# Performance work log

Measured on AMD Instinct MI355X. Metric: run time of the kernel, lower is better.

Reference implementation:

```python
import jax, jax.numpy as jnp
import numpy as np

NUM_EMBEDDINGS = 4096
EMBEDDING_DIM = 256
COMMITMENT_COST = 0.25
DECAY = 0.99
EPS = 1e-5
NORM_EPS = 1e-6
B, T = 64, 1024


def _l2norm(x):
    # torch.nn.functional.normalize: x / max(||x||_2, eps)
    n = jnp.sqrt(jnp.sum(x * x, axis=-1, keepdims=True))
    return x / jnp.maximum(n, NORM_EPS)


def setup_inputs() -> dict:
    key = jax.random.key(0)
    k1, k2 = jax.random.split(key)
    z = jax.random.normal(k1, (B, EMBEDDING_DIM, T), dtype=jnp.float32)
    weight = jax.random.normal(k2, (NUM_EMBEDDINGS, EMBEDDING_DIM), dtype=jnp.float32)
    weight = weight.at[0].set(0.0)  # reserved zero code
    ema_cluster_size = jnp.zeros((NUM_EMBEDDINGS,), dtype=jnp.float32)
    ema_w = weight  # buffer initialized as a clone of the codebook
    return {"z": z, "weight": weight, "ema_cluster_size": ema_cluster_size, "ema_w": ema_w}


def reference(z, weight, ema_cluster_size, ema_w):
    K = weight.shape[0]
    zp = jnp.transpose(z, (0, 2, 1))            # [B, T, D]
    b, t, d = zp.shape
    flat_z = zp.reshape(-1, d)                  # [N, D]
    flat_z_norm = _l2norm(flat_z)
    weight_norm = _l2norm(weight)
    # cosine similarity; argmin(1 - cos) == argmax(cos); code 0 excluded via -inf
    cos_sim = jnp.einsum('nd,kd->nk', flat_z_norm, weight_norm)
    cos_sim = cos_sim.at[:, 0].set(-jnp.inf)
    idx = jnp.argmax(cos_sim, axis=1)           # [N] int
    q = weight[idx].reshape(zp.shape)           # [B, T, D]

    # --- training-mode EMA codebook update (buffer math, no grad) ---
    counts = jax.ops.segment_sum(jnp.ones_like(idx, dtype=flat_z.dtype), idx, num_segments=K)
    new_cs = DECAY * ema_cluster_size + (1.0 - DECAY) * counts
    dw = jax.ops.segment_sum(flat_z_norm, idx, num_segments=K)  # [K, D]
    new_ema_w = DECAY * ema_w + (1.0 - DECAY) * dw
    new_cs = new_cs.at[0].set(0.0)
    new_ema_w = new_ema_w.at[0].set(0.0)
    n = jnp.sum(new_cs)
    cluster_size = (new_cs + EPS) / (n + K * EPS) * n
    new_weight = _l2norm(new_ema_w / cluster_size[:, None])
    new_weight = new_weight.at[0].set(0.0)

    loss = COMMITMENT_COST * jnp.mean((jax.lax.stop_gradient(q) - zp) ** 2)
    quantized = zp + jax.lax.stop_gradient(q - zp)  # straight-through
    quantized = jnp.transpose(quantized, (0, 2, 1))  # back to [B, D, T]
    codes = idx.reshape(b, t)
    return quantized, loss, codes, new_weight, new_cs, new_ema_w
```

## Files before the change

### kernel.cpp

```cpp
#include <hip/hip_runtime.h>
#include <math.h>

#define NUM_K 4096
#define DIM   256
#define TLEN  1024
#define DT    (DIM * TLEN)
#define CAP   2048

typedef short bf16x8 __attribute__((ext_vector_type(8)));
typedef float f32x4  __attribute__((ext_vector_type(4)));

static __device__ __forceinline__ unsigned short f2bf(float x) {
  unsigned u = __float_as_uint(x);
  u += 0x7fffu + ((u >> 16) & 1u);
  return (unsigned short)(u >> 16);
}

static __device__ __forceinline__ f32x4 mfma16(bf16x8 a, bf16x8 b, f32x4 c) {
  return __builtin_amdgcn_mfma_f32_16x16x32_bf16(a, b, c, 0, 0, 0);
}

__global__ __launch_bounds__(256) void wnorm_kernel(const float* __restrict__ w,
                                                    float* __restrict__ wnorms) {
  const int k = blockIdx.x * 256 + threadIdx.x;
  const float* row = w + (size_t)k * DIM;
  float p[2];
#pragma unroll
  for (int blk = 0; blk < 2; ++blk) {
    const float* b = row + blk * 128;
    float r[8];
#pragma unroll
    for (int j = 0; j < 8; ++j) r[j] = __fmul_rn(b[j], b[j]);
    for (int i = 8; i < 128; i += 8) {
#pragma unroll
      for (int j = 0; j < 8; ++j) r[j] = __fadd_rn(r[j], __fmul_rn(b[i + j], b[i + j]));
    }
    p[blk] = __fadd_rn(__fadd_rn(__fadd_rn(r[0], r[1]), __fadd_rn(r[2], r[3])),
                       __fadd_rn(__fadd_rn(r[4], r[5]), __fadd_rn(r[6], r[7])));
  }
  wnorms[k] = fmaxf(__fsqrt_rn(__fadd_rn(p[0], p[1])), 1e-6f);
}

__global__ __launch_bounds__(256) void wnf32_kernel(const float* __restrict__ w,
                                                    const float* __restrict__ wnorms,
                                                    float* __restrict__ wnf) {
  const int idx = blockIdx.x * 256 + threadIdx.x;
  const float m = wnorms[idx >> 6];
  const float4 v = *reinterpret_cast<const float4*>(w + (size_t)idx * 4);
  float4 o;
  o.x = __fdiv_rn(v.x, m); o.y = __fdiv_rn(v.y, m);
  o.z = __fdiv_rn(v.z, m); o.w = __fdiv_rn(v.w, m);
  *reinterpret_cast<float4*>(wnf + (size_t)idx * 4) = o;
}

__global__ __launch_bounds__(256) void wfrag_kernel(const float* __restrict__ wnf,
                                                    unsigned short* __restrict__ img) {
  const int t = blockIdx.x * 256 + threadIdx.x;
  const int lane = t & 63;
  const int fragid = t >> 6;
  const int jg = fragid & 3;
  const int kb = (fragid >> 2) & 7;
  const int chunk = fragid >> 5;
  const int c  = (chunk << 6) + (jg << 4) + (lane & 15);
  const int d0 = (kb << 5) + ((lane >> 4) << 3);
  const float* src = wnf + (size_t)c * DIM + d0;
  union { bf16x8 v; unsigned short u[8]; } o;
#pragma unroll
  for (int u = 0; u < 8; ++u) o.u[u] = f2bf(src[u]);
  *reinterpret_cast<bf16x8*>(img + (size_t)fragid * 512 + lane * 8) = o.v;
}

__global__ __launch_bounds__(256, 2) void vq_main_kernel(
    const float* __restrict__ z, const float* __restrict__ weight,
    const unsigned short* __restrict__ wimg, const float* __restrict__ wnf32,
    float* __restrict__ znT, float* __restrict__ out_codes,
    float* __restrict__ counts, float* __restrict__ loss_accum) {
  __shared__ float pp[2][64];
  __shared__ float tnorm[64];
  __shared__ float v1p[2][64];
  __shared__ float thr[64];
  __shared__ int   fidx[64];
  __shared__ int   clist[CAP];
  __shared__ float cscore[CAP];
  __shared__ int   ccount;

  const int tid  = threadIdx.x;
  const int bb   = blockIdx.x >> 4;
  const int t0   = (blockIdx.x & 15) << 6;
  const int lane = tid & 63;
  const int wv   = tid >> 6;
  const int wr   = wv >> 1;
  const int wc   = wv & 1;
  const float* zb = z + (size_t)bb * DT + t0;

  if (tid < 128) {
    const int tok = tid & 63, blk = tid >> 6;
    const float* zc = zb + tok;
    float r[8];
#pragma unroll
    for (int j = 0; j < 8; ++j) {
      const float v = zc[(size_t)(blk * 128 + j) * TLEN];
      r[j] = __fmul_rn(v, v);
    }
    for (int i = 8; i < 128; i += 8) {
#pragma unroll
      for (int j = 0; j < 8; ++j) {
        const float v = zc[(size_t)(blk * 128 + i + j) * TLEN];
        r[j] = __fadd_rn(r[j], __fmul_rn(v, v));
      }
    }
    pp[blk][tok] = __fadd_rn(__fadd_rn(__fadd_rn(r[0], r[1]), __fadd_rn(r[2], r[3])),
                             __fadd_rn(__fadd_rn(r[4], r[5]), __fadd_rn(r[6], r[7])));
  }
  if (tid == 0) ccount = 0;
  __syncthreads();
  if (tid < 64) tnorm[tid] = fmaxf(__fsqrt_rn(__fadd_rn(pp[0][tid], pp[1][tid])), 1e-6f);
  __syncthreads();

  {
    const int tok = tid & 63, seg = tid >> 6;
    const float m = tnorm[tok];
    const float* zc = zb + tok;
    float* orow = znT + (size_t)((bb << 10) + t0 + tok) * DIM + (seg << 6);
#pragma unroll 4
    for (int k4 = 0; k4 < 16; ++k4) {
      float4 o;
      o.x = __fdiv_rn(zc[(size_t)((seg << 6) + (k4 << 2) + 0) * TLEN], m);
      o.y = __fdiv_rn(zc[(size_t)((seg << 6) + (k4 << 2) + 1) * TLEN], m);
      o.z = __fdiv_rn(zc[(size_t)((seg << 6) + (k4 << 2) + 2) * TLEN], m);
      o.w = __fdiv_rn(zc[(size_t)((seg << 6) + (k4 << 2) + 3) * TLEN], m);
      *reinterpret_cast<float4*>(&orow[k4 << 2]) = o;
    }
  }

  bf16x8 afr[2][8];
  {
    const int tloc = (wr << 5) + (lane & 15);
    const int dr   = (lane >> 4) << 3;
#pragma unroll
    for (int i = 0; i < 2; ++i) {
      const float* zc = zb + tloc + (i << 4);
#pragma unroll
      for (int kb = 0; kb < 8; ++kb) {
        union { bf16x8 v; unsigned short u[8]; } a;
#pragma unroll
        for (int u = 0; u < 8; ++u)
          a.u[u] = f2bf(zc[(size_t)((kb << 5) + dr + u) * TLEN]);
        afr[i][kb] = a.v;
      }
    }
  }

  const unsigned short* bbase = wimg + (wc << 10) + (lane << 3);
  const f32x4 zero4 = {0.f, 0.f, 0.f, 0.f};
  const bool lc0 = (wc == 0) && ((lane & 15) == 0);

#define LOADC(buf, ch) do {                                              \
    const unsigned short* p_ = bbase + ((size_t)(ch) << 14);             \
    _Pragma("unroll")                                                    \
    for (int kb_ = 0; kb_ < 8; ++kb_) {                                  \
      buf[kb_]     = *reinterpret_cast<const bf16x8*>(p_ + (kb_ << 11)); \
      buf[kb_ + 8] = *reinterpret_cast<const bf16x8*>(p_ + (kb_ << 11) + 512); \
    }                                                                    \
    __builtin_amdgcn_sched_barrier(0);                                   \
  } while (0)

#define MFMAC(buf, accv) do {                                            \
    __builtin_amdgcn_s_setprio(1);                                       \
    _Pragma("unroll")                                                    \
    for (int kb_ = 0; kb_ < 8; ++kb_) {                                  \
      accv[0][0] = mfma16(afr[0][kb_], buf[kb_],     accv[0][0]);        \
      accv[1][0] = mfma16(afr[1][kb_], buf[kb_],     accv[1][0]);        \
      accv[0][1] = mfma16(afr[0][kb_], buf[kb_ + 8], accv[0][1]);        \
      accv[1][1] = mfma16(afr[1][kb_], buf[kb_ + 8], accv[1][1]);        \
    }                                                                    \
    __builtin_amdgcn_s_setprio(0);                                       \
  } while (0)

  float v1loc[2][4];
#pragma unroll
  for (int i = 0; i < 2; ++i)
#pragma unroll
    for (int r = 0; r < 4; ++r) v1loc[i][r] = -INFINITY;
  {
    bf16x8 bA[16], bB[16];
    LOADC(bA, 0);
#pragma unroll 1
    for (int chunk = 0; chunk < 64; chunk += 2) {
      LOADC(bB, chunk + 1);
      f32x4 acc[2][2];
      acc[0][0] = zero4; acc[0][1] = zero4; acc[1][0] = zero4; acc[1][1] = zero4;
      MFMAC(bA, acc);
      {
        const bool m0 = (chunk == 0) && lc0;
#pragma unroll
        for (int i = 0; i < 2; ++i)
#pragma unroll
          for (int r = 0; r < 4; ++r) {
            float v0 = acc[i][0][r];
            if (m0) v0 = -INFINITY;
            v1loc[i][r] = fmaxf(v1loc[i][r], fmaxf(v0, acc[i][1][r]));
          }
      }
      if (chunk + 2 < 64) LOADC(bA, chunk + 2);
      f32x4 ac2[2][2];
      ac2[0][0] = zero4; ac2[0][1] = zero4; ac2[1][0] = zero4; ac2[1][1] = zero4;
      MFMAC(bB, ac2);
#pragma unroll
      for (int i = 0; i < 2; ++i)
#pragma unroll
        for (int r = 0; r < 4; ++r)
          v1loc[i][r] = fmaxf(v1loc[i][r], fmaxf(ac2[i][0][r], ac2[i][1][r]));
    }
  }
#pragma unroll
  for (int i = 0; i < 2; ++i)
#pragma unroll
    for (int r = 0; r < 4; ++r) {
      float v = v1loc[i][r];
      v = fmaxf(v, __shfl_xor(v, 1));
      v = fmaxf(v, __shfl_xor(v, 2));
      v = fmaxf(v, __shfl_xor(v, 4));
      v = fmaxf(v, __shfl_xor(v, 8));
      if ((lane & 15) == 0)
        v1p[wc][(wr << 5) + (i << 4) + ((lane >> 4) << 2) + r] = v;
    }
  __syncthreads();
  if (tid < 64) thr[tid] = fmaxf(v1p[0][tid], v1p[1][tid]) - 0.02f * tnorm[tid];
  __syncthreads();

  float thrv_[2][4];
  {
    const int tb = (wr << 5) + ((lane >> 4) << 2);
#pragma unroll
    for (int i = 0; i < 2; ++i)
#pragma unroll
      for (int r = 0; r < 4; ++r) thrv_[i][r] = thr[tb + (i << 4) + r];
  }

  {
    bf16x8 bA[16], bB[16];
    LOADC(bA, 0);
#pragma unroll 1
    for (int chunk = 0; chunk < 64; chunk += 2) {
      LOADC(bB, chunk + 1);
      f32x4 acc[2][2];
      acc[0][0] = zero4; acc[0][1] = zero4; acc[1][0] = zero4; acc[1][1] = zero4;
      MFMAC(bA, acc);
#pragma unroll
      for (int i = 0; i < 2; ++i)
#pragma unroll
        for (int j = 0; j < 2; ++j) {
          const int c = (chunk << 6) + (wc << 5) + (j << 4) + (lane & 15);
#pragma unroll
          for (int r = 0; r < 4; ++r) {
            if (acc[i][j][r] >= thrv_[i][r] && c != 0) {
              const int pos = atomicAdd(&ccount, 1);
              if (pos < CAP)
                clist[pos] = (c << 7) | ((wr << 5) + (i << 4) + ((lane >> 4) << 2) + r);
            }
          }
        }
      if (chunk + 2 < 64) LOADC(bA, chunk + 2);
      f32x4 ac2[2][2];
      ac2[0][0] = zero4; ac2[0][1] = zero4; ac2[1][0] = zero4; ac2[1][1] = zero4;
      MFMAC(bB, ac2);
#pragma unroll
      for (int i = 0; i < 2; ++i)
#pragma unroll
        for (int j = 0; j < 2; ++j) {
          const int c = ((chunk + 1) << 6) + (wc << 5) + (j << 4) + (lane & 15);
#pragma unroll
          for (int r = 0; r < 4; ++r) {
            if (ac2[i][j][r] >= thrv_[i][r]) {
              const int pos = atomicAdd(&ccount, 1);
              if (pos < CAP)
                clist[pos] = (c << 7) | ((wr << 5) + (i << 4) + ((lane >> 4) << 2) + r);
            }
          }
        }
    }
  }
#undef LOADC
#undef MFMAC
  __syncthreads();

  const int ncand = min(ccount, CAP);
  for (int e = tid; e < ncand; e += 256) {
    const int pk = clist[e];
    const int tloc = pk & 127;
    const int c = pk >> 7;
    const float* za = znT + (size_t)((bb << 10) + t0 + tloc) * DIM;
    const float* wa = wnf32 + (size_t)c * DIM;
    float s = 0.f;
#pragma unroll 8
    for (int d = 0; d < DIM; ++d)
      s = fmaf(za[d], wa[d], s);
    cscore[e] = s;
  }
  __syncthreads();

  if (tid < 64) {
    float best = -INFINITY; int bc = NUM_K;
    for (int e = 0; e < ncand; ++e) {
      const int pk = clist[e];
      if ((pk & 127) == tid) {
        const float s = cscore[e]; const int c = pk >> 7;
        if (s > best || (s == best && c < bc)) { best = s; bc = c; }
      }
    }
    if (bc >= NUM_K) bc = 1;
    fidx[tid] = bc;
    out_codes[bb * TLEN + t0 + tid] = (float)bc;
    atomicAdd(&counts[bc], 1.0f);
  }
  __syncthreads();

  {
    float lpart = 0.f;
#pragma unroll 4
    for (int r = 0; r < 16; ++r) {
      const int tk = (r << 2) + wv;
      const int code = fidx[tk];
      const float* zc = zb + tk;
      const float4 w4 = *reinterpret_cast<const float4*>(
          weight + (size_t)code * DIM + (lane << 2));
      float4 zr4;
      zr4.x = zc[(size_t)((lane << 2) + 0) * TLEN];
      zr4.y = zc[(size_t)((lane << 2) + 1) * TLEN];
      zr4.z = zc[(size_t)((lane << 2) + 2) * TLEN];
      zr4.w = zc[(size_t)((lane << 2) + 3) * TLEN];
      const float dx = w4.x - zr4.x, dy = w4.y - zr4.y;
      const float dz = w4.z - zr4.z, dw_ = w4.w - zr4.w;
      lpart = fmaf(dx, dx, lpart); lpart = fmaf(dy, dy, lpart);
      lpart = fmaf(dz, dz, lpart); lpart = fmaf(dw_, dw_, lpart);
    }
#pragma unroll
    for (int off = 32; off; off >>= 1) lpart += __shfl_down(lpart, off, 64);
    if (lane == 0) atomicAdd(loss_accum, lpart);
  }
}

__global__ __launch_bounds__(256) void finalize_cs_kernel(
    const float* __restrict__ counts, const float* __restrict__ ema_cs,
    float* __restrict__ out_ncs, float* __restrict__ ws_n,
    const float* __restrict__ loss_accum, float* __restrict__ out_loss,
    int* __restrict__ offsets) {
  __shared__ float redf[4];
  __shared__ int   redi[4];
  const int tid = threadIdx.x;
  const int lane = tid & 63, wv = tid >> 6;
  const int base = tid << 4;
  int cloc[16]; int csum = 0; float fsum = 0.f;
#pragma unroll
  for (int j = 0; j < 16; ++j) {
    const int k = base + j;
    const float cf = counts[k];
    const float v = (k == 0) ? 0.f : 0.99f * ema_cs[k] + 0.01f * cf;
    out_ncs[k] = v; fsum += v;
    cloc[j] = csum; csum += (int)cf;
  }
  int inc = csum;
#pragma unroll
  for (int off = 1; off < 64; off <<= 1) {
    const int t = __shfl_up(inc, off, 64);
    if (lane >= off) inc += t;
  }
  float fs = fsum;
#pragma unroll
  for (int off = 32; off; off >>= 1) fs += __shfl_down(fs, off, 64);
  if (lane == 63) redi[wv] = inc;
  if (lane == 0)  redf[wv] = fs;
  __syncthreads();
  int wbase = 0;
#pragma unroll
  for (int w = 0; w < 4; ++w) wbase += (w < wv) ? redi[w] : 0;
  const int tbase = wbase + inc - csum;
#pragma unroll
  for (int j = 0; j < 16; ++j) offsets[base + j] = tbase + cloc[j];
  if (tid == 0) {
    ws_n[0] = redf[0] + redf[1] + redf[2] + redf[3];
    out_loss[0] = 0.25f * loss_accum[0] / 16777216.0f;
  }
}

__global__ __launch_bounds__(256) void scatter_kernel(
    const float* __restrict__ codes, const int* __restrict__ offsets,
    int* __restrict__ cursor, int* __restrict__ bucket) {
  const int g = blockIdx.x * 256 + threadIdx.x;
  const int c = (int)codes[g];
  const int pos = atomicAdd(&cursor[c], 1);
  bucket[offsets[c] + pos] = g;
}

__global__ __launch_bounds__(256) void dw_kernel(
    const float* __restrict__ znT, const float* __restrict__ counts,
    const int* __restrict__ offsets, const int* __restrict__ bucket,
    float* __restrict__ dw) {
  const int c = blockIdx.x;
  const int cnt = (int)counts[c];
  const int off = offsets[c];
  const int tid = threadIdx.x;
  float acc = 0.f;
  for (int i = 0; i < cnt; ++i) {
    const int g = bucket[off + i];
    acc += znT[(size_t)g * DIM + tid];
  }
  dw[(size_t)c * DIM + tid] = acc;
}

__global__ __launch_bounds__(256) void finalize_w_kernel(
    const float* __restrict__ ema_w, const float* __restrict__ ncs,
    const float* __restrict__ ws_n, float* __restrict__ new_ema_w,
    float* __restrict__ new_weight) {
  const int wid  = threadIdx.x >> 6;
  const int lane = threadIdx.x & 63;
  const int k    = (blockIdx.x << 2) + wid;
  const float n  = ws_n[0];
  const float cs = (ncs[k] + 1e-5f) / (n + 4096.0f * 1e-5f) * n;
  const float* erow = ema_w + k * DIM;
  float* nrow = new_ema_w + k * DIM;
  float* wrow = new_weight + k * DIM;
  const int d0 = lane << 2;
  float u[4]; float ss = 0.f;
#pragma unroll
  for (int j = 0; j < 4; ++j) {
    const float dwv = nrow[d0 + j];
    const float val = (k == 0) ? 0.f : 0.99f * erow[d0 + j] + 0.01f * dwv;
    nrow[d0 + j] = val;
    const float uu = val / cs;
    u[j] = uu;
    ss = fmaf(uu, uu, ss);
  }
#pragma unroll
  for (int off = 32; off; off >>= 1) ss += __shfl_xor(ss, off, 64);
  const float m = fmaxf(sqrtf(ss), 1e-6f);
#pragma unroll
  for (int j = 0; j < 4; ++j) wrow[d0 + j] = u[j] / m;
}

__global__ __launch_bounds__(256) void qwrite_kernel(
    const float* __restrict__ codes, const float* __restrict__ weight,
    float* __restrict__ out_q) {
  const int bb = blockIdx.x >> 4;
  const int t0 = (blockIdx.x & 15) << 6;
  const int ln = threadIdx.x & 63, qv = threadIdx.x >> 6;
  const int code = (int)codes[bb * TLEN + t0 + ln];
  const float* wrow = weight + (size_t)code * DIM;
  float* qb = out_q + (size_t)bb * DT + t0 + ln;
#pragma unroll 4
  for (int dd = 0; dd < 64; ++dd) {
    const int d = (qv << 6) + dd;
    qb[(size_t)d * TLEN] = wrow[d];
  }
}

extern "C" void kernel_launch(void* const* d_in, const int* in_sizes, int n_in,
                              void* d_out, int out_size, void* d_ws, size_t ws_size,
                              hipStream_t stream) {
  const float* z      = (const float*)d_in[0];
  const float* weight = (const float*)d_in[1];
  const float* ema_cs = (const float*)d_in[2];
  const float* ema_w  = (const float*)d_in[3];

  float* out = (float*)d_out;
  float* out_q     = out;
  float* out_loss  = out + 16777216;
  float* out_codes = out + 16777217;
  float* out_nw    = out + 16842753;
  float* out_ncs   = out + 17891329;
  float* out_new   = out + 17895425;

  float* counts     = (float*)d_ws;
  float* loss_accum = counts + 4096;
  float* ws_n       = counts + 4097;
  float* wnorms     = counts + 4352;

  unsigned short* wimg = (unsigned short*)(out_nw + 3);
  int* bucket  = (int*)(out_nw + 3);
  int* offsets = (int*)(out_nw + 524292);
  int* cursor  = (int*)(out_nw + 528388);
  float* wnf32 = out_new;

  hipMemsetAsync(d_ws, 0, 4098 * sizeof(float), stream);
  hipMemsetAsync(cursor, 0, 4096 * sizeof(int), stream);

  wnorm_kernel<<<16, 256, 0, stream>>>(weight, wnorms);
  wnf32_kernel<<<1024, 256, 0, stream>>>(weight, wnorms, wnf32);
  wfrag_kernel<<<512, 256, 0, stream>>>(wnf32, wimg);
  vq_main_kernel<<<1024, 256, 0, stream>>>(z, weight, wimg, wnf32, out_q ,
                                           out_codes, counts, loss_accum);
  finalize_cs_kernel<<<1, 256, 0, stream>>>(counts, ema_cs, out_ncs, ws_n,
                                            loss_accum, out_loss, offsets);
  scatter_kernel<<<256, 256, 0, stream>>>(out_codes, offsets, cursor, bucket);
  dw_kernel<<<NUM_K, 256, 0, stream>>>(out_q , counts, offsets, bucket, out_new);
  finalize_w_kernel<<<NUM_K / 4, 256, 0, stream>>>(ema_w, out_ncs, ws_n,
                                                   out_new, out_nw);
  qwrite_kernel<<<1024, 256, 0, stream>>>(out_codes, weight, out_q);
}
```

Before: 759.8 us.

## Fuse max and candidate passes into one single-pass MFMA sweep with running threshold

```diff
diff --git a/kernel.cpp b/kernel.cpp
--- a/kernel.cpp
+++ b/kernel.cpp
@@ -5,7 +5,7 @@
 #define DIM   256
 #define TLEN  1024
 #define DT    (DIM * TLEN)
-#define CAP   2048
+#define WCAP  1024
 
 typedef short bf16x8 __attribute__((ext_vector_type(8)));
 typedef float f32x4  __attribute__((ext_vector_type(4)));
@@ -18,6 +18,19 @@
 
 static __device__ __forceinline__ f32x4 mfma16(bf16x8 a, bf16x8 b, f32x4 c) {
   return __builtin_amdgcn_mfma_f32_16x16x32_bf16(a, b, c, 0, 0, 0);
+}
+
+static __device__ __forceinline__ float dppmax16(float v) {
+  int x = __float_as_int(v); int y;
+  y = __builtin_amdgcn_update_dpp(x, x, 0xB1, 0xF, 0xF, false);
+  v = fmaxf(v, __int_as_float(y)); x = __float_as_int(v);
+  y = __builtin_amdgcn_update_dpp(x, x, 0x4E, 0xF, 0xF, false);
+  v = fmaxf(v, __int_as_float(y)); x = __float_as_int(v);
+  y = __builtin_amdgcn_update_dpp(x, x, 0x141, 0xF, 0xF, false);
+  v = fmaxf(v, __int_as_float(y)); x = __float_as_int(v);
+  y = __builtin_amdgcn_update_dpp(x, x, 0x140, 0xF, 0xF, false);
+  v = fmaxf(v, __int_as_float(y));
+  return v;
 }
 
 __global__ __launch_bounds__(256) void wnorm_kernel(const float* __restrict__ w,
@@ -77,12 +90,10 @@
     float* __restrict__ counts, float* __restrict__ loss_accum) {
   __shared__ float pp[2][64];
   __shared__ float tnorm[64];
-  __shared__ float v1p[2][64];
-  __shared__ float thr[64];
   __shared__ int   fidx[64];
-  __shared__ int   clist[CAP];
-  __shared__ float cscore[CAP];
-  __shared__ int   ccount;
+  __shared__ int   clist[4][WCAP];
+  __shared__ int   wcnt[4];
+  __shared__ unsigned long long tokbest[64];
 
   const int tid  = threadIdx.x;
   const int bb   = blockIdx.x >> 4;
@@ -112,7 +123,8 @@
     pp[blk][tok] = __fadd_rn(__fadd_rn(__fadd_rn(r[0], r[1]), __fadd_rn(r[2], r[3])),
                              __fadd_rn(__fadd_rn(r[4], r[5]), __fadd_rn(r[6], r[7])));
   }
-  if (tid == 0) ccount = 0;
+  if (tid < 4)  wcnt[tid] = 0;
+  if (tid < 64) tokbest[tid] = 0ull;
   __syncthreads();
   if (tid < 64) tnorm[tid] = fmaxf(__fsqrt_rn(__fadd_rn(pp[0][tid], pp[1][tid])), 1e-6f);
   __syncthreads();
@@ -151,6 +163,15 @@
     }
   }
 
+  float wloc[2][4];
+  {
+    const int tb = (wr << 5) + ((lane >> 4) << 2);
+#pragma unroll
+    for (int i = 0; i < 2; ++i)
+#pragma unroll
+      for (int r = 0; r < 4; ++r) wloc[i][r] = 0.02f * tnorm[tb + (i << 4) + r];
+  }
+
   const unsigned short* bbase = wimg + (wc << 10) + (lane << 3);
   const f32x4 zero4 = {0.f, 0.f, 0.f, 0.f};
   const bool lc0 = (wc == 0) && ((lane & 15) == 0);
@@ -177,6 +198,35 @@
     __builtin_amdgcn_s_setprio(0);                                       \
   } while (0)
 
+#define PROCESS(accv, ch) do {                                           \
+    if ((ch) == 0 && lc0) {                                              \
+      _Pragma("unroll") for (int i_ = 0; i_ < 2; ++i_)                   \
+      _Pragma("unroll") for (int r_ = 0; r_ < 4; ++r_)                   \
+        accv[i_][0][r_] = -INFINITY;                                     \
+    }                                                                    \
+    _Pragma("unroll")                                                    \
+    for (int i_ = 0; i_ < 2; ++i_) {                                     \
+      _Pragma("unroll")                                                  \
+      for (int r_ = 0; r_ < 4; ++r_) {                                   \
+        float m_ = fmaxf(accv[i_][0][r_], accv[i_][1][r_]);              \
+        m_ = dppmax16(m_);                                               \
+        v1loc[i_][r_] = fmaxf(v1loc[i_][r_], m_);                        \
+        const float t_ = v1loc[i_][r_] - wloc[i_][r_];                   \
+        _Pragma("unroll")                                                \
+        for (int j_ = 0; j_ < 2; ++j_) {                                 \
+          if (accv[i_][j_][r_] >= t_) {                                  \
+            const int c_ = ((ch) << 6) + (wc << 5) + (j_ << 4) + (lane & 15); \
+            if (c_ != 0) {                                               \
+              const int pos_ = atomicAdd(&wcnt[wv], 1);                  \
+              if (pos_ < WCAP)                                           \
+                clist[wv][pos_] = (c_ << 6) | ((wr << 5) + (i_ << 4) + ((lane >> 4) << 2) + r_); \
+            }                                                            \
+          }                                                              \
+        }                                                                \
+      }                                                                  \
+    }                                                                    \
+  } while (0)
+
   float v1loc[2][4];
 #pragma unroll
   for (int i = 0; i < 2; ++i)
@@ -191,125 +241,44 @@
       f32x4 acc[2][2];
       acc[0][0] = zero4; acc[0][1] = zero4; acc[1][0] = zero4; acc[1][1] = zero4;
       MFMAC(bA, acc);
-      {
-        const bool m0 = (chunk == 0) && lc0;
-#pragma unroll
-        for (int i = 0; i < 2; ++i)
-#pragma unroll
-          for (int r = 0; r < 4; ++r) {
-            float v0 = acc[i][0][r];
-            if (m0) v0 = -INFINITY;
-            v1loc[i][r] = fmaxf(v1loc[i][r], fmaxf(v0, acc[i][1][r]));
-          }
-      }
+      PROCESS(acc, chunk);
       if (chunk + 2 < 64) LOADC(bA, chunk + 2);
       f32x4 ac2[2][2];
       ac2[0][0] = zero4; ac2[0][1] = zero4; ac2[1][0] = zero4; ac2[1][1] = zero4;
       MFMAC(bB, ac2);
-#pragma unroll
-      for (int i = 0; i < 2; ++i)
-#pragma unroll
-        for (int r = 0; r < 4; ++r)
-          v1loc[i][r] = fmaxf(v1loc[i][r], fmaxf(ac2[i][0][r], ac2[i][1][r]));
-    }
-  }
-#pragma unroll
-  for (int i = 0; i < 2; ++i)
-#pragma unroll
-    for (int r = 0; r < 4; ++r) {
-      float v = v1loc[i][r];
-      v = fmaxf(v, __shfl_xor(v, 1));
-      v = fmaxf(v, __shfl_xor(v, 2));
-      v = fmaxf(v, __shfl_xor(v, 4));
-      v = fmaxf(v, __shfl_xor(v, 8));
-      if ((lane & 15) == 0)
-        v1p[wc][(wr << 5) + (i << 4) + ((lane >> 4) << 2) + r] = v;
-    }
-  __syncthreads();
-  if (tid < 64) thr[tid] = fmaxf(v1p[0][tid], v1p[1][tid]) - 0.02f * tnorm[tid];
-  __syncthreads();
-
-  float thrv_[2][4];
-  {
-    const int tb = (wr << 5) + ((lane >> 4) << 2);
-#pragma unroll
-    for (int i = 0; i < 2; ++i)
-#pragma unroll
-      for (int r = 0; r < 4; ++r) thrv_[i][r] = thr[tb + (i << 4) + r];
-  }
-
-  {
-    bf16x8 bA[16], bB[16];
-    LOADC(bA, 0);
-#pragma unroll 1
-    for (int chunk = 0; chunk < 64; chunk += 2) {
-      LOADC(bB, chunk + 1);
-      f32x4 acc[2][2];
-      acc[0][0] = zero4; acc[0][1] = zero4; acc[1][0] = zero4; acc[1][1] = zero4;
-      MFMAC(bA, acc);
-#pragma unroll
-      for (int i = 0; i < 2; ++i)
-#pragma unroll
-        for (int j = 0; j < 2; ++j) {
-          const int c = (chunk << 6) + (wc << 5) + (j << 4) + (lane & 15);
-#pragma unroll
-          for (int r = 0; r < 4; ++r) {
-            if (acc[i][j][r] >= thrv_[i][r] && c != 0) {
-              const int pos = atomicAdd(&ccount, 1);
-              if (pos < CAP)
-                clist[pos] = (c << 7) | ((wr << 5) + (i << 4) + ((lane >> 4) << 2) + r);
-            }
-          }
-        }
-      if (chunk + 2 < 64) LOADC(bA, chunk + 2);
-      f32x4 ac2[2][2];
-      ac2[0][0] = zero4; ac2[0][1] = zero4; ac2[1][0] = zero4; ac2[1][1] = zero4;
-      MFMAC(bB, ac2);
-#pragma unroll
-      for (int i = 0; i < 2; ++i)
-#pragma unroll
-        for (int j = 0; j < 2; ++j) {
-          const int c = ((chunk + 1) << 6) + (wc << 5) + (j << 4) + (lane & 15);
-#pragma unroll
-          for (int r = 0; r < 4; ++r) {
-            if (ac2[i][j][r] >= thrv_[i][r]) {
-              const int pos = atomicAdd(&ccount, 1);
-              if (pos < CAP)
-                clist[pos] = (c << 7) | ((wr << 5) + (i << 4) + ((lane >> 4) << 2) + r);
-            }
-          }
-        }
+      PROCESS(ac2, chunk + 1);
     }
   }
 #undef LOADC
 #undef MFMAC
-  __syncthreads();
-
-  const int ncand = min(ccount, CAP);
-  for (int e = tid; e < ncand; e += 256) {
-    const int pk = clist[e];
-    const int tloc = pk & 127;
-    const int c = pk >> 7;
-    const float* za = znT + (size_t)((bb << 10) + t0 + tloc) * DIM;
-    const float* wa = wnf32 + (size_t)c * DIM;
-    float s = 0.f;
+#undef PROCESS
+  __syncthreads();
+
+#pragma unroll 1
+  for (int w = 0; w < 4; ++w) {
+    const int n = min(wcnt[w], WCAP);
+    for (int e = tid; e < n; e += 256) {
+      const int pk = clist[w][e];
+      const int tloc = pk & 63;
+      const int c = pk >> 6;
+      const float* za = znT + (size_t)((bb << 10) + t0 + tloc) * DIM;
+      const float* wa = wnf32 + (size_t)c * DIM;
+      float s = 0.f;
 #pragma unroll 8
-    for (int d = 0; d < DIM; ++d)
-      s = fmaf(za[d], wa[d], s);
-    cscore[e] = s;
+      for (int d = 0; d < DIM; ++d)
+        s = fmaf(za[d], wa[d], s);
+      unsigned uk = __float_as_uint(s);
+      uk = (uk & 0x80000000u) ? ~uk : (uk | 0x80000000u);
+      const unsigned long long key =
+          ((unsigned long long)uk << 32) | (unsigned)(4095 - c);
+      atomicMax(&tokbest[tloc], key);
+    }
   }
   __syncthreads();
 
   if (tid < 64) {
-    float best = -INFINITY; int bc = NUM_K;
-    for (int e = 0; e < ncand; ++e) {
-      const int pk = clist[e];
-      if ((pk & 127) == tid) {
-        const float s = cscore[e]; const int c = pk >> 7;
-        if (s > best || (s == best && c < bc)) { best = s; bc = c; }
-      }
-    }
-    if (bc >= NUM_K) bc = 1;
+    const unsigned long long key = tokbest[tid];
+    const int bc = 4095 - (int)(key & 0xFFFull);
     fidx[tid] = bc;
     out_codes[bb * TLEN + t0 + tid] = (float)bc;
     atomicAdd(&counts[bc], 1.0f);
```

Result: slower. 896.0 us (+17.9%).
